# Optimization experiments

Hardware: AMD Instinct MI355X
Metric: run time of the kernel (lower is better)

Reference implementation:

```python
import jax, jax.numpy as jnp
import numpy as np

B, N, D = 4, 4096, 768
H, DH = 12, 64          # heads, dim_head; inner_dim = H*DH = D
DEPTH = 4
HID = int(D * 4.0)      # mlp hidden
LN_EPS = 1e-5


def setup_inputs() -> dict:
    key = jax.random.key(0)
    ks = jax.random.split(key, 7)
    s = 0.02
    return {
        "x": jax.random.normal(ks[0], (B, N, D), jnp.float32),
        "ln1_g": jnp.ones((DEPTH, D), jnp.float32),
        "ln1_b": jnp.zeros((DEPTH, D), jnp.float32),
        "qkv_w": jax.random.normal(ks[1], (DEPTH, D, H * DH), jnp.float32) * s,
        "temp": jnp.ones((DEPTH, H, 1), jnp.float32),
        "out_w": jax.random.normal(ks[2], (DEPTH, H * DH, D), jnp.float32) * s,
        "out_b": jnp.zeros((DEPTH, D), jnp.float32),
        "ln2_g": jnp.ones((DEPTH, D), jnp.float32),
        "ln2_b": jnp.zeros((DEPTH, D), jnp.float32),
        "fc1_w": jax.random.normal(ks[3], (DEPTH, D, HID), jnp.float32) * s,
        "fc1_b": jnp.zeros((DEPTH, HID), jnp.float32),
        "fc2_w": jax.random.normal(ks[4], (DEPTH, HID, D), jnp.float32) * s,
        "fc2_b": jnp.zeros((DEPTH, D), jnp.float32),
    }


def _layernorm(x, g, b):
    mu = jnp.mean(x, axis=-1, keepdims=True)
    var = jnp.mean((x - mu) ** 2, axis=-1, keepdims=True)
    return (x - mu) * jax.lax.rsqrt(var + LN_EPS) * g + b


def _tss_attention(h, qkv_w, temp, out_w, out_b):
    b, n, d = h.shape
    w = h @ qkv_w                                   # (b, n, H*DH)
    w = w.reshape(b, n, H, DH).transpose(0, 2, 1, 3)  # (b, h, n, d)
    # F.normalize over token dim (dim=-2), eps=1e-12
    nrm = jnp.sqrt(jnp.sum(w * w, axis=2, keepdims=True))
    w_normed = w / jnp.maximum(nrm, 1e-12)
    logits = jnp.sum(w_normed * w_normed, axis=-1) * temp[None]  # (b, h, n)
    Pi = jax.nn.softmax(logits, axis=-1)
    Pi_n = Pi / (jnp.sum(Pi, axis=-1, keepdims=True) + 1e-8)
    dots = jnp.einsum('bhn,bhnd->bhd', Pi_n, w * w)[:, :, None, :]  # (b, h, 1, d)
    attn = 1.0 / (1.0 + dots)
    out = -(w * Pi[..., None]) * attn               # (b, h, n, d)
    out = out.transpose(0, 2, 1, 3).reshape(b, n, H * DH)
    return out @ out_w + out_b


def reference(x, ln1_g, ln1_b, qkv_w, temp, out_w, out_b,
              ln2_g, ln2_b, fc1_w, fc1_b, fc2_w, fc2_b):
    for i in range(DEPTH):
        h = _layernorm(x, ln1_g[i], ln1_b[i])
        x = _tss_attention(h, qkv_w[i], temp[i], out_w[i], out_b[i]) + x
        h2 = _layernorm(x, ln2_g[i], ln2_b[i])
        mlp = jax.nn.gelu(h2 @ fc1_w[i] + fc1_b[i], approximate=False) @ fc2_w[i] + fc2_b[i]
        x = mlp + x
    return x
```

## Files before the change

kernel.cpp:

```cpp
#include <hip/hip_runtime.h>
#include <cstdint>
#include <cstddef>

static constexpr int Bc = 4, Nc = 4096, Dc = 768, Hc = 12, DHc = 64;
static constexpr int HIDc = 3072, DEPTHc = 4;
static constexpr int Mc = Bc * Nc;
static constexpr int BHc = Bc * Hc;
static constexpr int BHDc = BHc * DHc;

typedef unsigned short u16;
typedef __bf16 bf16x8 __attribute__((ext_vector_type(8)));
typedef float  f32x4  __attribute__((ext_vector_type(4)));

#define DEV __device__ __forceinline__

DEV u16 f2bf(float x) {
    uint32_t u = __float_as_uint(x);
    u += 0x7fffu + ((u >> 16) & 1u);
    return (u16)(u >> 16);
}
DEV float bf2f(u16 u) { return __uint_as_float(((uint32_t)u) << 16); }
DEV void unp2(uint32_t u, float& a, float& b) {
    a = __uint_as_float(u << 16);
    b = __uint_as_float(u & 0xffff0000u);
}
DEV float gelu_fast(float x) {
    float y = 0.7978845608f * (x + 0.044715f * x * x * x);
    float e = __expf(2.0f * y);
    float t = 1.0f - 2.0f / (e + 1.0f);
    return 0.5f * x * (1.0f + t);
}

DEV void ldg_lds16(const void* g, void* l) {
    __builtin_amdgcn_global_load_lds(
        (const __attribute__((address_space(1))) uint32_t*)(uintptr_t)g,
        (__attribute__((address_space(3))) uint32_t*)(uint32_t)(uintptr_t)l,
        16, 0, 0);
}

__global__ void detect_kernel(const uint32_t* __restrict__ x, uint32_t* __restrict__ flag) {
    int t = threadIdx.x;
    uint32_t w = x[t];
    int e = (w >> 7) & 0xFF;
    __shared__ int cnt[256];
    cnt[t] = (e >= 100 && e <= 140) ? 1 : 0;
    __syncthreads();
    for (int s = 128; s; s >>= 1) {
        if (t < s) cnt[t] += cnt[t + s];
        __syncthreads();
    }
    if (t == 0) flag[0] = (cnt[0] >= 128) ? 1u : 0u;
}

__global__ __launch_bounds__(256) void sentinel_kernel(u16* __restrict__ out, int n) {
    int i = blockIdx.x * 256 + threadIdx.x;
    if (i < n) out[i] = 0x449A;
}

__global__ __launch_bounds__(256) void cvt_param_kernel(
    const void* __restrict__ src, float* __restrict__ dst, int n,
    const uint32_t* __restrict__ flag) {
    int i = blockIdx.x * 256 + threadIdx.x;
    if (i >= n) return;
    if (flag[0]) dst[i] = bf2f(((const u16*)src)[i]);
    else         dst[i] = ((const float*)src)[i];
}

__global__ __launch_bounds__(256) void transpose_cvt_off(
    const void* __restrict__ src, size_t eoff, u16* __restrict__ dst,
    int R, int C, const uint32_t* __restrict__ flag) {
    __shared__ u16 tile[32][33];
    const bool isbf = (flag[0] != 0);
    int c0 = blockIdx.x * 32, r0 = blockIdx.y * 32;
    int tx = threadIdx.x & 31, ty = threadIdx.x >> 5;
#pragma unroll
    for (int j = 0; j < 32; j += 8) {
        size_t off = eoff + (size_t)(r0 + ty + j) * C + (c0 + tx);
        tile[ty + j][tx] = isbf ? ((const u16*)src)[off] : f2bf(((const float*)src)[off]);
    }
    __syncthreads();
#pragma unroll
    for (int j = 0; j < 32; j += 8)
        dst[(size_t)(c0 + ty + j) * R + (r0 + tx)] = tile[tx][ty + j];
}

__global__ __launch_bounds__(256) void ln_kernel(
    const float* __restrict__ x, const float* __restrict__ g,
    const float* __restrict__ bta, u16* __restrict__ out) {
    int row = blockIdx.x, t = threadIdx.x;
    const float* xr = x + (size_t)row * Dc;
    float v0 = xr[t], v1 = xr[t + 256], v2 = xr[t + 512];
    float s = v0 + v1 + v2;
    float ss = v0 * v0 + v1 * v1 + v2 * v2;
    __shared__ float red[8];
    for (int m = 32; m; m >>= 1) { s += __shfl_xor(s, m, 64); ss += __shfl_xor(ss, m, 64); }
    int wave = t >> 6, lane = t & 63;
    if (lane == 0) { red[wave] = s; red[4 + wave] = ss; }
    __syncthreads();
    s  = red[0] + red[1] + red[2] + red[3];
    ss = red[4] + red[5] + red[6] + red[7];
    float mu = s * (1.0f / Dc);
    float var = ss * (1.0f / Dc) - mu * mu;
    float rs = rsqrtf(var + 1e-5f);
    u16* orow = out + (size_t)row * Dc;
    orow[t]       = f2bf((v0 - mu) * rs * g[t]       + bta[t]);
    orow[t + 256] = f2bf((v1 - mu) * rs * g[t + 256] + bta[t + 256]);
    orow[t + 512] = f2bf((v2 - mu) * rs * g[t + 512] + bta[t + 512]);
}

template <int MODE>
__global__ __launch_bounds__(256) void gemm_kernel(
    const u16* __restrict__ A, const u16* __restrict__ Bt,
    float* Cf, u16* Cb, const float* __restrict__ bias, const float* res,
    float* aux, int M, int N, int K) {
    __shared__ __attribute__((aligned(16))) u16 As[128 * 32];
    __shared__ __attribute__((aligned(16))) u16 Bs[128 * 32];
    const int tid = threadIdx.x;
    const int wave = tid >> 6, lane = tid & 63;
    const int bm = blockIdx.y * 128, bn = blockIdx.x * 128;
    const int wm = (wave >> 1) * 64, wn = (wave & 1) * 64;

    const int srow = wave * 16 + (lane >> 2);
    const int skel = (((lane & 3) ^ ((lane >> 3) & 3)) * 8);
    const u16* a0 = A  + (size_t)(bm + srow) * K + skel;
    const u16* a1 = a0 + (size_t)64 * K;
    const u16* b0 = Bt + (size_t)(bn + srow) * K + skel;
    const u16* b1 = b0 + (size_t)64 * K;
    u16* lA0 = As + wave * 512;
    u16* lA1 = As + 2048 + wave * 512;
    u16* lB0 = Bs + wave * 512;
    u16* lB1 = Bs + 2048 + wave * 512;

    f32x4 acc[4][4] = {};
    const int fm = lane & 15;
    const int c  = lane >> 4;
    const int fs = (fm >> 1) & 3;
    const int fko = ((c ^ fs) * 8);

    for (int k0 = 0; k0 < K; k0 += 32) {
        ldg_lds16(a0 + k0, lA0);
        ldg_lds16(a1 + k0, lA1);
        ldg_lds16(b0 + k0, lB0);
        ldg_lds16(b1 + k0, lB1);
        __syncthreads();
        bf16x8 af[4], bfr[4];
#pragma unroll
        for (int i = 0; i < 4; i++) {
            af[i]  = *(const bf16x8*)(As + (wm + i * 16 + fm) * 32 + fko);
            bfr[i] = *(const bf16x8*)(Bs + (wn + i * 16 + fm) * 32 + fko);
        }
#pragma unroll
        for (int mi = 0; mi < 4; mi++)
#pragma unroll
            for (int ni = 0; ni < 4; ni++)
                acc[mi][ni] = __builtin_amdgcn_mfma_f32_16x16x32_bf16(
                    af[mi], bfr[ni], acc[mi][ni], 0, 0, 0);
        __syncthreads();
    }

    const int er = (lane >> 4) * 4;
    const int ec = lane & 15;
    float csq[4] = {0.f, 0.f, 0.f, 0.f};
#pragma unroll
    for (int mi = 0; mi < 4; mi++) {
        const int row0 = bm + wm + mi * 16 + er;
#pragma unroll
        for (int ni = 0; ni < 4; ni++) {
            const int col = bn + wn + ni * 16 + ec;
#pragma unroll
            for (int r = 0; r < 4; r++) {
                const size_t off = (size_t)(row0 + r) * N + col;
                float v = acc[mi][ni][r];
                if (MODE == 1) {
                    Cf[off] = v + bias[col] + res[off];
                } else if (MODE == 2) {
                    Cb[off] = f2bf(gelu_fast(v + bias[col]));
                } else {
                    Cb[off] = f2bf(v);
                    csq[ni] += v * v;
                }
            }
        }
    }
    if (MODE == 3) {
        const int b = bm >> 12;
#pragma unroll
        for (int ni = 0; ni < 4; ni++) {
            float s = csq[ni];
            s += __shfl_xor(s, 16, 64);
            s += __shfl_xor(s, 32, 64);
            if (lane < 16) {
                const int col = bn + wn + ni * 16 + lane;
                const int bh = b * Hc + (col >> 6);
                atomicAdd(&aux[bh * DHc + (col & 63)], s);
            }
        }
    }
}

__global__ __launch_bounds__(256) void logits_kernel(
    const u16* __restrict__ w, const float* __restrict__ nrm2,
    const float* __restrict__ tp, float* __restrict__ logits) {
    int blk = blockIdx.x;
    int chunk = blk & 15, bh = blk >> 4;
    int b = bh / Hc, h = bh - b * Hc;
    int t = threadIdx.x, dq = t & 3, nr = t >> 2;
    __shared__ float inv[64];
    if (t < 64) inv[t] = 1.0f / fmaxf(nrm2[bh * DHc + t], 1e-24f);
    __syncthreads();
    float tl = tp[h];
#pragma unroll
    for (int jj = 0; jj < 4; jj++) {
        int n = chunk * 256 + jj * 64 + nr;
        const uint4* wr = (const uint4*)(w + ((size_t)b * Nc + n) * Dc + h * DHc + dq * 16);
        uint4 u0 = wr[0], u1 = wr[1];
        float acc = 0.f;
        float e0, e1;
        const float* iv = inv + dq * 16;
        unp2(u0.x, e0, e1); acc += e0 * e0 * iv[0]  + e1 * e1 * iv[1];
        unp2(u0.y, e0, e1); acc += e0 * e0 * iv[2]  + e1 * e1 * iv[3];
        unp2(u0.z, e0, e1); acc += e0 * e0 * iv[4]  + e1 * e1 * iv[5];
        unp2(u0.w, e0, e1); acc += e0 * e0 * iv[6]  + e1 * e1 * iv[7];
        unp2(u1.x, e0, e1); acc += e0 * e0 * iv[8]  + e1 * e1 * iv[9];
        unp2(u1.y, e0, e1); acc += e0 * e0 * iv[10] + e1 * e1 * iv[11];
        unp2(u1.z, e0, e1); acc += e0 * e0 * iv[12] + e1 * e1 * iv[13];
        unp2(u1.w, e0, e1); acc += e0 * e0 * iv[14] + e1 * e1 * iv[15];
        acc += __shfl_xor(acc, 1, 64);
        acc += __shfl_xor(acc, 2, 64);
        if (dq == 0) logits[(size_t)bh * Nc + n] = tl * acc;
    }
}

__global__ __launch_bounds__(256) void softmax_kernel(
    const float* __restrict__ logits, float* __restrict__ Pi, float* __restrict__ rowsc) {
    int bh = blockIdx.x, t = threadIdx.x;
    int wave = t >> 6, lane = t & 63;
    const float4* lg = (const float4*)(logits + (size_t)bh * Nc);
    float4 v[4];
    float mx = -3.4e38f;
    __shared__ float red[4];
#pragma unroll
    for (int j = 0; j < 4; j++) {
        v[j] = lg[t + 256 * j];
        mx = fmaxf(mx, fmaxf(fmaxf(v[j].x, v[j].y), fmaxf(v[j].z, v[j].w)));
    }
    for (int m = 32; m; m >>= 1) mx = fmaxf(mx, __shfl_xor(mx, m, 64));
    if (lane == 0) red[wave] = mx;
    __syncthreads();
    mx = fmaxf(fmaxf(red[0], red[1]), fmaxf(red[2], red[3]));
    __syncthreads();
    float s = 0.f;
#pragma unroll
    for (int j = 0; j < 4; j++) {
        v[j].x = expf(v[j].x - mx); v[j].y = expf(v[j].y - mx);
        v[j].z = expf(v[j].z - mx); v[j].w = expf(v[j].w - mx);
        s += v[j].x + v[j].y + v[j].z + v[j].w;
    }
    for (int m = 32; m; m >>= 1) s += __shfl_xor(s, m, 64);
    if (lane == 0) red[wave] = s;
    __syncthreads();
    s = red[0] + red[1] + red[2] + red[3];
    __syncthreads();
    float invs = 1.0f / s;
    float s2 = 0.f;
    float4* Pr = (float4*)(Pi + (size_t)bh * Nc);
#pragma unroll
    for (int j = 0; j < 4; j++) {
        float4 p;
        p.x = v[j].x * invs; p.y = v[j].y * invs;
        p.z = v[j].z * invs; p.w = v[j].w * invs;
        s2 += p.x + p.y + p.z + p.w;
        Pr[t + 256 * j] = p;
    }
    for (int m = 32; m; m >>= 1) s2 += __shfl_xor(s2, m, 64);
    if (lane == 0) red[wave] = s2;
    __syncthreads();
    if (t == 0) rowsc[bh] = 1.0f / (red[0] + red[1] + red[2] + red[3] + 1e-8f);
}

__global__ __launch_bounds__(256) void dots_kernel(
    const u16* __restrict__ w, const float* __restrict__ Pi,
    const float* __restrict__ rowsc, float* __restrict__ dots) {
    int blk = blockIdx.x;
    int chunk = blk & 15, bh = blk >> 4;
    int b = bh / Hc, h = bh - b * Hc;
    int t = threadIdx.x, d4 = t & 15, rg = t >> 4;
    const u16* base = w + ((size_t)b * Nc + chunk * 256 + rg) * Dc + h * DHc + d4 * 4;
    const float* Prow = Pi + (size_t)bh * Nc + chunk * 256 + rg;
    float4 acc = {0.f, 0.f, 0.f, 0.f};
#pragma unroll 4
    for (int j = 0; j < 16; j++) {
        uint2 u = *(const uint2*)(base + (size_t)j * 16 * Dc);
        float p = Prow[j * 16];
        float a0, a1, a2, a3;
        unp2(u.x, a0, a1); unp2(u.y, a2, a3);
        acc.x += p * a0 * a0; acc.y += p * a1 * a1;
        acc.z += p * a2 * a2; acc.w += p * a3 * a3;
    }
    __shared__ float4 red[256];
    red[t] = acc;
    __syncthreads();
    if (t < 64) {
        float s = 0.f;
#pragma unroll
        for (int r = 0; r < 16; r++) {
            const float* f = (const float*)&red[r * 16 + (t >> 2)];
            s += f[t & 3];
        }
        atomicAdd(&dots[bh * DHc + t], s * rowsc[bh]);
    }
}

__global__ __launch_bounds__(256) void attnout_kernel(
    const u16* __restrict__ w, const float* __restrict__ Pi,
    const float* __restrict__ dots, u16* __restrict__ out) {
    int idx = blockIdx.x * 256 + threadIdx.x;
    int cg = idx % (Dc / 8);
    int m = idx / (Dc / 8);
    int b = m >> 12, n = m & 4095;
    int c = cg * 8, h = c >> 6, d = c & 63;
    int bh = b * Hc + h;
    uint4 wv = ((const uint4*)w)[idx];
    float pi = Pi[(size_t)bh * Nc + n];
    float4 dv0 = *(const float4*)(dots + bh * DHc + d);
    float4 dv1 = *(const float4*)(dots + bh * DHc + d + 4);
    float a0, a1, a2, a3, a4, a5, a6, a7;
    unp2(wv.x, a0, a1); unp2(wv.y, a2, a3);
    unp2(wv.z, a4, a5); unp2(wv.w, a6, a7);
    union { u16 u[8]; uint4 v4; } pk;
    pk.u[0] = f2bf(-(a0 * pi) / (1.0f + dv0.x));
    pk.u[1] = f2bf(-(a1 * pi) / (1.0f + dv0.y));
    pk.u[2] = f2bf(-(a2 * pi) / (1.0f + dv0.z));
    pk.u[3] = f2bf(-(a3 * pi) / (1.0f + dv0.w));
    pk.u[4] = f2bf(-(a4 * pi) / (1.0f + dv1.x));
    pk.u[5] = f2bf(-(a5 * pi) / (1.0f + dv1.y));
    pk.u[6] = f2bf(-(a6 * pi) / (1.0f + dv1.z));
    pk.u[7] = f2bf(-(a7 * pi) / (1.0f + dv1.w));
    ((uint4*)out)[idx] = pk.v4;
}

extern "C" void kernel_launch(void* const* d_in, const int* in_sizes, int n_in,
                              void* d_out, int out_size, void* d_ws, size_t ws_size,
                              hipStream_t stream) {
    const void* x_in = d_in[0];
    const void* ln1g = d_in[1];
    const void* ln1b = d_in[2];
    const void* qkvw = d_in[3];
    const void* temp = d_in[4];
    const void* outw = d_in[5];
    const void* outb = d_in[6];
    const void* ln2g = d_in[7];
    const void* ln2b = d_in[8];
    const void* fc1w = d_in[9];
    const void* fc1b = d_in[10];
    const void* fc2w = d_in[11];
    const void* fc2b = d_in[12];

    char* p = (char*)d_ws;
    auto alloc = [&](size_t bytes) {
        void* r = (void*)p;
        p += (bytes + 255) & ~(size_t)255;
        return r;
    };
    float* xbuf = (float*)alloc((size_t)Mc * Dc * 4);
    void*  big  = alloc((size_t)Mc * HIDc * 2);
    u16*   wbuf = (u16*)big;
    u16*   gbuf = (u16*)big;
    u16*  abuf  = (u16*)alloc((size_t)Mc * Dc * 2);
    const size_t QKV_T = (size_t)Dc * Dc, OUT_T = (size_t)Dc * Dc;
    const size_t FC1_T = (size_t)HIDc * Dc, FC2_T = (size_t)Dc * HIDc;
    const size_t LSTRIDE = QKV_T + OUT_T + FC1_T + FC2_T;
    u16*  wTL   = (u16*)alloc(LSTRIDE * 2);
    float* nrm2 = (float*)alloc((size_t)BHDc * 4);
    float* dots = (float*)alloc((size_t)BHDc * 4);
    float* logit = (float*)alloc((size_t)BHc * Nc * 4);
    float* Pi    = (float*)alloc((size_t)BHc * Nc * 4);
    float* rowsc = (float*)alloc((size_t)BHc * 4);
    uint32_t* flag = (uint32_t*)alloc(256);
    float* ln1g_f = (float*)alloc((size_t)DEPTHc * Dc * 4);
    float* ln1b_f = (float*)alloc((size_t)DEPTHc * Dc * 4);
    float* ln2g_f = (float*)alloc((size_t)DEPTHc * Dc * 4);
    float* ln2b_f = (float*)alloc((size_t)DEPTHc * Dc * 4);
    float* outb_f = (float*)alloc((size_t)DEPTHc * Dc * 4);
    float* fc1b_f = (float*)alloc((size_t)DEPTHc * HIDc * 4);
    float* fc2b_f = (float*)alloc((size_t)DEPTHc * Dc * 4);
    float* temp_f = (float*)alloc((size_t)DEPTHc * Hc * 4);
    if ((size_t)(p - (char*)d_ws) > ws_size) {
        sentinel_kernel<<<(out_size + 255) / 256, 256, 0, stream>>>((u16*)d_out, out_size);
        return;
    }

    detect_kernel<<<1, 256, 0, stream>>>((const uint32_t*)x_in, flag);

    auto cvt = [&](const void* s, float* d, int n) {
        cvt_param_kernel<<<(n + 255) / 256, 256, 0, stream>>>(s, d, n, flag);
    };
    cvt(x_in, xbuf, Mc * Dc);
    cvt(ln1g, ln1g_f, DEPTHc * Dc);
    cvt(ln1b, ln1b_f, DEPTHc * Dc);
    cvt(ln2g, ln2g_f, DEPTHc * Dc);
    cvt(ln2b, ln2b_f, DEPTHc * Dc);
    cvt(outb, outb_f, DEPTHc * Dc);
    cvt(fc1b, fc1b_f, DEPTHc * HIDc);
    cvt(fc2b, fc2b_f, DEPTHc * Dc);
    cvt(temp, temp_f, DEPTHc * Hc);

    u16* qkvT = wTL;
    u16* outT = qkvT + QKV_T;
    u16* fc1T = outT + OUT_T;
    u16* fc2T = fc1T + FC1_T;

    for (int i = 0; i < DEPTHc; i++) {
        transpose_cvt_off<<<dim3(Dc / 32, Dc / 32), 256, 0, stream>>>(
            qkvw, (size_t)i * Dc * Dc, qkvT, Dc, Dc, flag);
        transpose_cvt_off<<<dim3(Dc / 32, Dc / 32), 256, 0, stream>>>(
            outw, (size_t)i * Dc * Dc, outT, Dc, Dc, flag);
        transpose_cvt_off<<<dim3(HIDc / 32, Dc / 32), 256, 0, stream>>>(
            fc1w, (size_t)i * Dc * HIDc, fc1T, Dc, HIDc, flag);
        transpose_cvt_off<<<dim3(Dc / 32, HIDc / 32), 256, 0, stream>>>(
            fc2w, (size_t)i * HIDc * Dc, fc2T, HIDc, Dc, flag);

        ln_kernel<<<Mc, 256, 0, stream>>>(xbuf, ln1g_f + i * Dc, ln1b_f + i * Dc, abuf);
        hipMemsetAsync(nrm2, 0, (size_t)2 * BHDc * 4, stream);
        gemm_kernel<3><<<dim3(Dc / 128, Mc / 128), 256, 0, stream>>>(
            abuf, qkvT, nullptr, wbuf, nullptr, nullptr, nrm2, Mc, Dc, Dc);
        logits_kernel<<<BHc * 16, 256, 0, stream>>>(wbuf, nrm2, temp_f + i * Hc, logit);
        softmax_kernel<<<BHc, 256, 0, stream>>>(logit, Pi, rowsc);
        dots_kernel<<<BHc * 16, 256, 0, stream>>>(wbuf, Pi, rowsc, dots);
        attnout_kernel<<<(Mc * Dc / 8) / 256, 256, 0, stream>>>(wbuf, Pi, dots, abuf);
        gemm_kernel<1><<<dim3(Dc / 128, Mc / 128), 256, 0, stream>>>(
            abuf, outT, xbuf, nullptr, outb_f + i * Dc, xbuf, nullptr, Mc, Dc, Dc);
        ln_kernel<<<Mc, 256, 0, stream>>>(xbuf, ln2g_f + i * Dc, ln2b_f + i * Dc, abuf);
        gemm_kernel<2><<<dim3(HIDc / 128, Mc / 128), 256, 0, stream>>>(
            abuf, fc1T, nullptr, gbuf, fc1b_f + i * HIDc, nullptr, nullptr, Mc, HIDc, Dc);
        gemm_kernel<1><<<dim3(Dc / 128, Mc / 128), 256, 0, stream>>>(
            gbuf, fc2T, xbuf, nullptr, fc2b_f + i * Dc, xbuf, nullptr, Mc, Dc, HIDc);
    }
    hipMemcpyAsync(d_out, xbuf, (size_t)Mc * Dc * 4, hipMemcpyDeviceToDevice, stream);
}
```

Before: 1.856 ms.

## Rewrite GEMM as 256x256 tile with 4-stage LDS ring and split-phase MFMA

Replaces the 128x128, single-buffered GEMM with a 256x256 tile run by 8 waves. It uses a 4-deep LDS ring buffer where the loads for tile t+2 are issued while tile t is computed. The MFMA work is split into two halves separated by barriers, with setprio raised during compute, to overlap global-to-LDS traffic with matrix math and raise arithmetic intensity. In exchange it uses much more LDS (128KB per block) and more accumulator registers. It also gives far fewer blocks for the N=768 GEMMs (3x64 = 192 blocks), which may underfill the 256 CUs.

```diff
diff --git a/kernel.cpp b/kernel.cpp
--- a/kernel.cpp
+++ b/kernel.cpp
@@ -109,75 +109,112 @@
 }
 
 template <int MODE>
-__global__ __launch_bounds__(256) void gemm_kernel(
+__global__ __launch_bounds__(512, 2) void gemm_kernel(
     const u16* __restrict__ A, const u16* __restrict__ Bt,
     float* Cf, u16* Cb, const float* __restrict__ bias, const float* res,
     float* aux, int M, int N, int K) {
-    __shared__ __attribute__((aligned(16))) u16 As[128 * 32];
-    __shared__ __attribute__((aligned(16))) u16 Bs[128 * 32];
+    __shared__ __attribute__((aligned(16))) u16 lds[4][2][256 * 32];
     const int tid = threadIdx.x;
     const int wave = tid >> 6, lane = tid & 63;
-    const int bm = blockIdx.y * 128, bn = blockIdx.x * 128;
-    const int wm = (wave >> 1) * 64, wn = (wave & 1) * 64;
-
-    const int srow = wave * 16 + (lane >> 2);
-    const int skel = (((lane & 3) ^ ((lane >> 3) & 3)) * 8);
-    const u16* a0 = A  + (size_t)(bm + srow) * K + skel;
-    const u16* a1 = a0 + (size_t)64 * K;
-    const u16* b0 = Bt + (size_t)(bn + srow) * K + skel;
-    const u16* b1 = b0 + (size_t)64 * K;
-    u16* lA0 = As + wave * 512;
-    u16* lA1 = As + 2048 + wave * 512;
-    u16* lB0 = Bs + wave * 512;
-    u16* lB1 = Bs + 2048 + wave * 512;
-
-    f32x4 acc[4][4] = {};
+    const int wm = wave >> 2, wn = wave & 3;
+    const int bm = blockIdx.y * 256, bn = blockIdx.x * 256;
+    const int NT = K >> 5;
+
+    const int srow   = lane >> 2;
+    const int schunk = (lane & 3) ^ ((lane >> 3) & 3);
+    const u16* ag = A  + (size_t)(bm + wave * 16 + srow) * K + schunk * 8;
+    const u16* bg = Bt + (size_t)(bn + wave * 16 + srow) * K + schunk * 8;
+    const size_t rstep = (size_t)128 * K;
+
+    auto stA = [&](int t) {
+        u16* d = &lds[t & 3][0][wave * 512];
+        const u16* g = ag + (size_t)t * 32;
+        ldg_lds16(g, d);
+        ldg_lds16(g + rstep, d + 4096);
+    };
+    auto stB = [&](int t) {
+        u16* d = &lds[t & 3][1][wave * 512];
+        const u16* g = bg + (size_t)t * 32;
+        ldg_lds16(g, d);
+        ldg_lds16(g + rstep, d + 4096);
+    };
+
     const int fm = lane & 15;
-    const int c  = lane >> 4;
-    const int fs = (fm >> 1) & 3;
-    const int fko = ((c ^ fs) * 8);
-
-    for (int k0 = 0; k0 < K; k0 += 32) {
-        ldg_lds16(a0 + k0, lA0);
-        ldg_lds16(a1 + k0, lA1);
-        ldg_lds16(b0 + k0, lB0);
-        ldg_lds16(b1 + k0, lB1);
-        __syncthreads();
-        bf16x8 af[4], bfr[4];
-#pragma unroll
-        for (int i = 0; i < 4; i++) {
-            af[i]  = *(const bf16x8*)(As + (wm + i * 16 + fm) * 32 + fko);
-            bfr[i] = *(const bf16x8*)(Bs + (wn + i * 16 + fm) * 32 + fko);
-        }
-#pragma unroll
-        for (int mi = 0; mi < 4; mi++)
-#pragma unroll
-            for (int ni = 0; ni < 4; ni++)
-                acc[mi][ni] = __builtin_amdgcn_mfma_f32_16x16x32_bf16(
-                    af[mi], bfr[ni], acc[mi][ni], 0, 0, 0);
-        __syncthreads();
+    const int fc = lane >> 4;
+    const int fp = fc ^ ((fm >> 1) & 3);
+    const int aoff = (wm * 128 + fm) * 32 + fp * 8;
+    const int boff = (wn * 64  + fm) * 32 + fp * 8;
+
+    f32x4 acc[8][4] = {};
+
+    stA(0); stB(0); stA(1); stB(1);
+    asm volatile("s_waitcnt vmcnt(4)" ::: "memory");
+    __builtin_amdgcn_s_barrier();
+    __builtin_amdgcn_sched_barrier(0);
+
+    for (int t = 0; t < NT; ++t) {
+        const int tb = t & 3;
+        const u16* Ab = &lds[tb][0][0];
+        const u16* Bb = &lds[tb][1][0];
+        bf16x8 af[8], bq[4];
+#pragma unroll
+        for (int mf = 0; mf < 8; ++mf)
+            af[mf] = *(const bf16x8*)(Ab + aoff + mf * 512);
+        bq[0] = *(const bf16x8*)(Bb + boff);
+        bq[1] = *(const bf16x8*)(Bb + boff + 512);
+        if (t + 2 < NT) stA(t + 2);
+        __builtin_amdgcn_s_barrier();
+        __builtin_amdgcn_sched_barrier(0);
+        __builtin_amdgcn_s_setprio(1);
+#pragma unroll
+        for (int mf = 0; mf < 8; ++mf) {
+            acc[mf][0] = __builtin_amdgcn_mfma_f32_16x16x32_bf16(af[mf], bq[0], acc[mf][0], 0, 0, 0);
+            acc[mf][1] = __builtin_amdgcn_mfma_f32_16x16x32_bf16(af[mf], bq[1], acc[mf][1], 0, 0, 0);
+        }
+        __builtin_amdgcn_s_setprio(0);
+        __builtin_amdgcn_s_barrier();
+        __builtin_amdgcn_sched_barrier(0);
+        bq[2] = *(const bf16x8*)(Bb + boff + 1024);
+        bq[3] = *(const bf16x8*)(Bb + boff + 1536);
+        if (t + 2 < NT) {
+            stB(t + 2);
+            asm volatile("s_waitcnt vmcnt(4)" ::: "memory");
+        } else if (t + 1 < NT) {
+            asm volatile("s_waitcnt vmcnt(0)" ::: "memory");
+        }
+        __builtin_amdgcn_s_barrier();
+        __builtin_amdgcn_sched_barrier(0);
+        __builtin_amdgcn_s_setprio(1);
+#pragma unroll
+        for (int mf = 0; mf < 8; ++mf) {
+            acc[mf][2] = __builtin_amdgcn_mfma_f32_16x16x32_bf16(af[mf], bq[2], acc[mf][2], 0, 0, 0);
+            acc[mf][3] = __builtin_amdgcn_mfma_f32_16x16x32_bf16(af[mf], bq[3], acc[mf][3], 0, 0, 0);
+        }
+        __builtin_amdgcn_s_setprio(0);
+        __builtin_amdgcn_s_barrier();
+        __builtin_amdgcn_sched_barrier(0);
     }
 
     const int er = (lane >> 4) * 4;
     const int ec = lane & 15;
     float csq[4] = {0.f, 0.f, 0.f, 0.f};
 #pragma unroll
-    for (int mi = 0; mi < 4; mi++) {
-        const int row0 = bm + wm + mi * 16 + er;
-#pragma unroll
-        for (int ni = 0; ni < 4; ni++) {
-            const int col = bn + wn + ni * 16 + ec;
-#pragma unroll
-            for (int r = 0; r < 4; r++) {
+    for (int mf = 0; mf < 8; ++mf) {
+        const int row0 = bm + wm * 128 + mf * 16 + er;
+#pragma unroll
+        for (int nf = 0; nf < 4; ++nf) {
+            const int col = bn + wn * 64 + nf * 16 + ec;
+#pragma unroll
+            for (int r = 0; r < 4; ++r) {
                 const size_t off = (size_t)(row0 + r) * N + col;
-                float v = acc[mi][ni][r];
+                float v = acc[mf][nf][r];
                 if (MODE == 1) {
                     Cf[off] = v + bias[col] + res[off];
                 } else if (MODE == 2) {
                     Cb[off] = f2bf(gelu_fast(v + bias[col]));
                 } else {
                     Cb[off] = f2bf(v);
-                    csq[ni] += v * v;
+                    csq[nf] += v * v;
                 }
             }
         }
@@ -185,12 +222,12 @@
     if (MODE == 3) {
         const int b = bm >> 12;
 #pragma unroll
-        for (int ni = 0; ni < 4; ni++) {
-            float s = csq[ni];
+        for (int nf = 0; nf < 4; ++nf) {
+            float s = csq[nf];
             s += __shfl_xor(s, 16, 64);
             s += __shfl_xor(s, 32, 64);
             if (lane < 16) {
-                const int col = bn + wn + ni * 16 + lane;
+                const int col = bn + wn * 64 + nf * 16 + lane;
                 const int bh = b * Hc + (col >> 6);
                 atomicAdd(&aux[bh * DHc + (col & 63)], s);
             }
@@ -422,18 +459,18 @@
 
         ln_kernel<<<Mc, 256, 0, stream>>>(xbuf, ln1g_f + i * Dc, ln1b_f + i * Dc, abuf);
         hipMemsetAsync(nrm2, 0, (size_t)2 * BHDc * 4, stream);
-        gemm_kernel<3><<<dim3(Dc / 128, Mc / 128), 256, 0, stream>>>(
+        gemm_kernel<3><<<dim3(Dc / 256, Mc / 256), 512, 0, stream>>>(
             abuf, qkvT, nullptr, wbuf, nullptr, nullptr, nrm2, Mc, Dc, Dc);
         logits_kernel<<<BHc * 16, 256, 0, stream>>>(wbuf, nrm2, temp_f + i * Hc, logit);
         softmax_kernel<<<BHc, 256, 0, stream>>>(logit, Pi, rowsc);
         dots_kernel<<<BHc * 16, 256, 0, stream>>>(wbuf, Pi, rowsc, dots);
         attnout_kernel<<<(Mc * Dc / 8) / 256, 256, 0, stream>>>(wbuf, Pi, dots, abuf);
-        gemm_kernel<1><<<dim3(Dc / 128, Mc / 128), 256, 0, stream>>>(
+        gemm_kernel<1><<<dim3(Dc / 256, Mc / 256), 512, 0, stream>>>(
             abuf, outT, xbuf, nullptr, outb_f + i * Dc, xbuf, nullptr, Mc, Dc, Dc);
         ln_kernel<<<Mc, 256, 0, stream>>>(xbuf, ln2g_f + i * Dc, ln2b_f + i * Dc, abuf);
-        gemm_kernel<2><<<dim3(HIDc / 128, Mc / 128), 256, 0, stream>>>(
+        gemm_kernel<2><<<dim3(HIDc / 256, Mc / 256), 512, 0, stream>>>(
             abuf, fc1T, nullptr, gbuf, fc1b_f + i * HIDc, nullptr, nullptr, Mc, HIDc, Dc);
-        gemm_kernel<1><<<dim3(Dc / 128, Mc / 128), 256, 0, stream>>>(
+        gemm_kernel<1><<<dim3(Dc / 256, Mc / 256), 512, 0, stream>>>(
             gbuf, fc2T, xbuf, nullptr, fc2b_f + i * Dc, xbuf, nullptr, Mc, Dc, HIDc);
     }
     hipMemcpyAsync(d_out, xbuf, (size_t)Mc * Dc * 4, hipMemcpyDeviceToDevice, stream);
```

Result: faster. 1.709 ms (-7.9%).
